# Optimization experiments

Hardware: AMD Instinct MI355X
Metric: run time of the kernel (lower is better)

## Reference

```python
import jax, jax.numpy as jnp
import numpy as np
import math

CAPACITY_FACTOR = 1.0

def setup_inputs() -> dict:
    key = jax.random.key(0)
    k1, k2 = jax.random.split(key)
    x = jax.random.normal(k1, (8192, 2048), dtype=jnp.float32)
    wg = jax.random.normal(k2, (64, 2048), dtype=jnp.float32) * (1.0 / np.sqrt(2048))
    return {"x": x, "wg": wg}

def reference(x, wg):
    # logits = Linear(model_dim, num_experts, bias=False)(x)
    logits = jnp.einsum('sd,ed->se', x, wg)
    gates = jax.nn.softmax(logits, axis=1)  # [s, e]
    s, e = gates.shape
    capacity = math.ceil(s / e * CAPACITY_FACTOR)  # static
    indices1_s = jnp.argmax(gates, axis=1)  # [s]
    mask1 = jax.nn.one_hot(indices1_s, e, dtype=jnp.int32)  # [s, e]
    locations1 = jnp.cumsum(mask1, axis=0) - 1  # position within each expert queue
    # aux load-balancing loss
    me = jnp.mean(gates, axis=0)
    ce = jnp.mean(mask1.astype(gates.dtype), axis=0)
    l_aux = jnp.mean(me * ce) * (e * e)
    # drop tokens over capacity
    mask1 = mask1 * (locations1 < capacity).astype(jnp.int32)
    locations1_s = jnp.sum(locations1 * mask1, axis=1)  # [s] int
    mask1_float = mask1.astype(gates.dtype)
    gates1_s = jnp.sum(gates * mask1_float, axis=1)  # 'se,se->s'
    gates1 = gates1_s[:, None] * mask1_float         # 's,se->se'
    locations1_sc = jax.nn.one_hot(locations1_s, capacity, dtype=gates.dtype)  # [s, c]
    combine_weights = gates1[:, :, None] * locations1_sc[:, None, :]  # 'se,sc->sec'
    dispatch_mask = combine_weights.astype(bool)
    return l_aux, combine_weights, dispatch_mask
```

## Files before the change

### kernel.cpp

```cpp
#include <hip/hip_runtime.h>
#include <cstdint>
#include <cstddef>


#define S_TOK 8192
#define NEXP 64
#define DIM 2048
#define CAP 128
#define COMB_ELEMS ((size_t)S_TOK * NEXP * CAP)
#define OUT_ELEMS (1 + 2 * COMB_ELEMS)
#define NQUAD (OUT_ELEMS / 4)

#define TOK_TILE 128
#define NSLICE 4
#define KSLICE (DIM / NSLICE)
#define KC 32

#define GEMM_BLKS 256
#define ZERO_BLKS 768
#define TOTAL_BLKS (GEMM_BLKS + ZERO_BLKS)
#define QCHUNK 43691

__global__ __launch_bounds__(256, 4) void fused_zero_gemm(
    const float* __restrict__ x, const float* __restrict__ wg,
    float* __restrict__ P, float* __restrict__ gsum,
    float* __restrict__ out)
{
    const int tid = threadIdx.x;

    if (blockIdx.x >= GEMM_BLKS) {
        const int zb = blockIdx.x - GEMM_BLKS;
        size_t begin = (size_t)zb * QCHUNK;
        size_t end   = begin + QCHUNK;
        if (end > (size_t)NQUAD) end = (size_t)NQUAD;
        const float4 z = { 0.0f, 0.0f, 0.0f, 0.0f };
        for (size_t q = begin + tid; q < end; q += 256)
            *(float4*)(out + 4 * q) = z;
        if (zb == 0 && tid == 0) out[OUT_ELEMS - 1] = 0.0f;
        return;
    }

    __shared__ float xs[KC][132];
    __shared__ float wsh[KC][68];

    const int tile  = blockIdx.x >> 2;
    const int slice = blockIdx.x & 3;
    const int tok0 = tile * TOK_TILE;
    const int k0   = slice * KSLICE;

    if (blockIdx.x == 0 && tid < NEXP) gsum[tid] = 0.0f;

    const int tt = tid >> 4;
    const int te = tid & 15;

    float acc[8][4];
#pragma unroll
    for (int i = 0; i < 8; ++i)
#pragma unroll
        for (int j = 0; j < 4; ++j) acc[i][j] = 0.0f;

    const int we  = tid & 63;
    const int wkq = tid >> 6;

    float4 xv[4], wv[2];
#pragma unroll
    for (int r = 0; r < 4; ++r) {
        int idx = tid + 256 * r;
        int t = idx >> 3, kq = idx & 7;
        xv[r] = *(const float4*)(x + (size_t)(tok0 + t) * DIM + k0 + 4 * kq);
    }
    wv[0] = *(const float4*)(wg + (size_t)we * DIM + k0 + 4 * wkq);
    wv[1] = *(const float4*)(wg + (size_t)we * DIM + k0 + 4 * (wkq + 4));

    for (int kc = 0; kc < KSLICE; kc += KC) {
        __syncthreads();
#pragma unroll
        for (int r = 0; r < 4; ++r) {
            int idx = tid + 256 * r;
            int t = idx >> 3, k4 = (idx & 7) * 4;
            xs[k4 + 0][t] = xv[r].x; xs[k4 + 1][t] = xv[r].y;
            xs[k4 + 2][t] = xv[r].z; xs[k4 + 3][t] = xv[r].w;
        }
        {
            int k4 = 4 * wkq;
            wsh[k4 + 0][we] = wv[0].x; wsh[k4 + 1][we] = wv[0].y;
            wsh[k4 + 2][we] = wv[0].z; wsh[k4 + 3][we] = wv[0].w;
            int k4b = k4 + 16;
            wsh[k4b + 0][we] = wv[1].x; wsh[k4b + 1][we] = wv[1].y;
            wsh[k4b + 2][we] = wv[1].z; wsh[k4b + 3][we] = wv[1].w;
        }
        __syncthreads();
        if (kc + KC < KSLICE) {
#pragma unroll
            for (int r = 0; r < 4; ++r) {
                int idx = tid + 256 * r;
                int t = idx >> 3, kq = idx & 7;
                xv[r] = *(const float4*)(x + (size_t)(tok0 + t) * DIM + k0 + kc + KC + 4 * kq);
            }
            wv[0] = *(const float4*)(wg + (size_t)we * DIM + k0 + kc + KC + 4 * wkq);
            wv[1] = *(const float4*)(wg + (size_t)we * DIM + k0 + kc + KC + 4 * (wkq + 4));
        }
#pragma unroll 8
        for (int k = 0; k < KC; ++k) {
            float4 a0 = *(const float4*)&xs[k][8 * tt];
            float4 a1 = *(const float4*)&xs[k][8 * tt + 4];
            float4 b  = *(const float4*)&wsh[k][4 * te];
            const float* ap0 = &a0.x; const float* ap1 = &a1.x; const float* bp = &b.x;
#pragma unroll
            for (int i = 0; i < 4; ++i)
#pragma unroll
                for (int j = 0; j < 4; ++j) {
                    acc[i][j]     += ap0[i] * bp[j];
                    acc[i + 4][j] += ap1[i] * bp[j];
                }
        }
    }

#pragma unroll
    for (int i = 0; i < 8; ++i) {
        size_t off = ((size_t)slice * S_TOK + tok0 + 8 * tt + i) * NEXP + 4 * te;
        float4 v = { acc[i][0], acc[i][1], acc[i][2], acc[i][3] };
        *(float4*)(P + off) = v;
    }
}

__global__ __launch_bounds__(256) void reduce_kernel(
    const float* __restrict__ P,
    int* __restrict__ idx_out, float* __restrict__ gate_out,
    float* __restrict__ gsum)
{
    __shared__ float sme[NEXP];
    const int tid = threadIdx.x;
    const int tok0 = blockIdx.x * 32;
    const int ty = tid >> 5;
    const int tx = tid & 31;
    const int t0 = ty * 4;
    const int e0 = tx * 2;

    if (tid < NEXP) sme[tid] = 0.0f;

    float gm0 = 0.0f, gm1 = 0.0f;
#pragma unroll
    for (int i = 0; i < 4; ++i) {
        int tok = tok0 + t0 + i;
        float l0 = 0.0f, l1 = 0.0f;
#pragma unroll
        for (int s = 0; s < NSLICE; ++s) {
            float2 p = *(const float2*)&P[((size_t)s * S_TOK + tok) * NEXP + e0];
            l0 += p.x; l1 += p.y;
        }
        float v; int ix;
        if (l1 > l0) { v = l1; ix = e0 + 1; } else { v = l0; ix = e0; }
#pragma unroll
        for (int off = 16; off; off >>= 1) {
            float ov = __shfl_xor(v, off, 32);
            int   oi = __shfl_xor(ix, off, 32);
            if (ov > v || (ov == v && oi < ix)) { v = ov; ix = oi; }
        }
        float z0 = __expf(l0 - v), z1 = __expf(l1 - v);
        float zs = z0 + z1;
#pragma unroll
        for (int off = 16; off; off >>= 1) zs += __shfl_xor(zs, off, 32);
        float inv = 1.0f / zs;
        gm0 += z0 * inv; gm1 += z1 * inv;
        if (tx == 0) {
            idx_out[tok]  = ix;
            gate_out[tok] = inv;
        }
    }
    atomicAdd(&sme[e0], gm0);
    atomicAdd(&sme[e0 + 1], gm1);
    __syncthreads();
    if (tid < NEXP) atomicAdd(&gsum[tid], sme[tid]);
}

__global__ __launch_bounds__(1024) void scan_scatter(
    const int* __restrict__ idx, const float* __restrict__ gate,
    const float* __restrict__ gsum, float* __restrict__ out)
{
    __shared__ int wavecnt[16][NEXP];
    __shared__ int basecnt[NEXP];
    const int tid  = threadIdx.x;
    const int lane = tid & 63;
    const int wv   = tid >> 6;

    if (tid < NEXP) basecnt[tid] = 0;
    __syncthreads();

    for (int it = 0; it < S_TOK / 1024; ++it) {
        int tok = it * 1024 + tid;
        int e = idx[tok];
        unsigned long long m = ~0ull, lm = ~0ull;
#pragma unroll
        for (int b = 0; b < 6; ++b) {
            unsigned long long bal = __ballot((e >> b) & 1);
            m  &= ((e >> b) & 1)    ? bal : ~bal;
            lm &= ((lane >> b) & 1) ? bal : ~bal;
        }
        int rank = __popcll(m & ((1ull << lane) - 1ull));
        wavecnt[wv][lane] = __popcll(lm);
        __syncthreads();
        int off = 0;
        for (int w = 0; w < wv; ++w) off += wavecnt[w][e];
        int loc = basecnt[e] + off + rank;
        if (loc < CAP) {
            size_t base = 1 + (size_t)tok * (NEXP * CAP) + (size_t)e * CAP + loc;
            out[base] = gate[tok];
            out[base + COMB_ELEMS] = 1.0f;
        }
        __syncthreads();
        if (tid < NEXP) {
            int tot = 0;
#pragma unroll
            for (int w = 0; w < 16; ++w) tot += wavecnt[w][tid];
            basecnt[tid] += tot;
        }
        __syncthreads();
    }

    if (tid < NEXP) {
        float p = gsum[tid] * (float)basecnt[tid];
#pragma unroll
        for (int off = 32; off; off >>= 1) p += __shfl_xor(p, off, 64);
        if (tid == 0) out[0] = p * 9.5367431640625e-07f;
    }
}

extern "C" void kernel_launch(void* const* d_in, const int* in_sizes, int n_in,
                              void* d_out, int out_size, void* d_ws, size_t ws_size,
                              hipStream_t stream) {
    const float* x  = (const float*)d_in[0];
    const float* wg = (const float*)d_in[1];
    float* out = (float*)d_out;

    int*   idx  = (int*)d_ws;
    float* gate = (float*)((char*)d_ws + 32768);
    float* gsum = (float*)((char*)d_ws + 65536);
    float* P    = (float*)((char*)d_ws + 262144);

    fused_zero_gemm<<<TOTAL_BLKS, 256, 0, stream>>>(x, wg, P, gsum, out);
    reduce_kernel<<<S_TOK / 32, 256, 0, stream>>>(P, idx, gate, gsum);
    scan_scatter<<<1, 1024, 0, stream>>>(idx, gate, gsum, out);
}
```

Measured before the change: 615.6 us.

## Spread output zeroing across all three kernels and split scatter out of scan

The large output memset was done only inside the GEMM kernel. It is now split into three ranges, each handled by extra blocks in the gemm, reduce and scan kernels, so the zero-fill overlaps the small compute stages, including the single-block scan. The scan now writes per-token locations to workspace, and a separate scatter kernel writes the nonzero entries after all zeroing has finished. This removes the ordering hazard between zeroing and scattering, at the cost of one more launch and a small extra buffer.

```diff
diff --git a/kernel.cpp b/kernel.cpp
--- a/kernel.cpp
+++ b/kernel.cpp
@@ -9,33 +9,36 @@
 #define CAP 128
 #define COMB_ELEMS ((size_t)S_TOK * NEXP * CAP)
 #define OUT_ELEMS (1 + 2 * COMB_ELEMS)
-#define NQUAD (OUT_ELEMS / 4)
+#define NQUAD ((size_t)(OUT_ELEMS / 4))
+
+#define QA ((size_t)14000000)
+#define QB ((size_t)24000000)
 
 #define TOK_TILE 128
 #define NSLICE 4
 #define KSLICE (DIM / NSLICE)
 #define KC 32
 
-#define GEMM_BLKS 256
-#define ZERO_BLKS 768
-#define TOTAL_BLKS (GEMM_BLKS + ZERO_BLKS)
-#define QCHUNK 43691
-
-__global__ __launch_bounds__(256, 4) void fused_zero_gemm(
+__device__ __forceinline__ void zero_quads(float* __restrict__ out,
+                                           size_t q_begin, size_t q_end,
+                                           int nblocks, int bid) {
+    const float4 z = { 0.0f, 0.0f, 0.0f, 0.0f };
+    size_t stride = (size_t)nblocks * blockDim.x;
+    for (size_t q = q_begin + (size_t)bid * blockDim.x + threadIdx.x;
+         q < q_end; q += stride)
+        *(float4*)(out + 4 * q) = z;
+}
+
+__global__ __launch_bounds__(256, 4) void gemm_zero_a(
     const float* __restrict__ x, const float* __restrict__ wg,
     float* __restrict__ P, float* __restrict__ gsum,
     float* __restrict__ out)
 {
     const int tid = threadIdx.x;
 
-    if (blockIdx.x >= GEMM_BLKS) {
-        const int zb = blockIdx.x - GEMM_BLKS;
-        size_t begin = (size_t)zb * QCHUNK;
-        size_t end   = begin + QCHUNK;
-        if (end > (size_t)NQUAD) end = (size_t)NQUAD;
-        const float4 z = { 0.0f, 0.0f, 0.0f, 0.0f };
-        for (size_t q = begin + tid; q < end; q += 256)
-            *(float4*)(out + 4 * q) = z;
+    if (blockIdx.x >= 256) {
+        const int zb = blockIdx.x - 256;
+        zero_quads(out, 0, QA, 768, zb);
         if (zb == 0 && tid == 0) out[OUT_ELEMS - 1] = 0.0f;
         return;
     }
@@ -124,13 +127,19 @@
     }
 }
 
-__global__ __launch_bounds__(256) void reduce_kernel(
+__global__ __launch_bounds__(256) void reduce_zero_b(
     const float* __restrict__ P,
     int* __restrict__ idx_out, float* __restrict__ gate_out,
-    float* __restrict__ gsum)
-{
+    float* __restrict__ gsum, float* __restrict__ out)
+{
+    const int tid = threadIdx.x;
+
+    if (blockIdx.x >= 256) {
+        zero_quads(out, QA, QB, 768, blockIdx.x - 256);
+        return;
+    }
+
     __shared__ float sme[NEXP];
-    const int tid = threadIdx.x;
     const int tok0 = blockIdx.x * 32;
     const int ty = tid >> 5;
     const int tx = tid & 31;
@@ -174,13 +183,19 @@
     if (tid < NEXP) atomicAdd(&gsum[tid], sme[tid]);
 }
 
-__global__ __launch_bounds__(1024) void scan_scatter(
-    const int* __restrict__ idx, const float* __restrict__ gate,
-    const float* __restrict__ gsum, float* __restrict__ out)
-{
+__global__ __launch_bounds__(1024) void scan_zero_c(
+    const int* __restrict__ idx, const float* __restrict__ gsum,
+    int* __restrict__ loc_out, float* __restrict__ out)
+{
+    const int tid = threadIdx.x;
+
+    if (blockIdx.x > 0) {
+        zero_quads(out, QB, NQUAD, 256, (int)blockIdx.x - 1);
+        return;
+    }
+
     __shared__ int wavecnt[16][NEXP];
     __shared__ int basecnt[NEXP];
-    const int tid  = threadIdx.x;
     const int lane = tid & 63;
     const int wv   = tid >> 6;
 
@@ -202,12 +217,7 @@
         __syncthreads();
         int off = 0;
         for (int w = 0; w < wv; ++w) off += wavecnt[w][e];
-        int loc = basecnt[e] + off + rank;
-        if (loc < CAP) {
-            size_t base = 1 + (size_t)tok * (NEXP * CAP) + (size_t)e * CAP + loc;
-            out[base] = gate[tok];
-            out[base + COMB_ELEMS] = 1.0f;
-        }
+        loc_out[tok] = basecnt[e] + off + rank;
         __syncthreads();
         if (tid < NEXP) {
             int tot = 0;
@@ -223,6 +233,19 @@
 #pragma unroll
         for (int off = 32; off; off >>= 1) p += __shfl_xor(p, off, 64);
         if (tid == 0) out[0] = p * 9.5367431640625e-07f;
+    }
+}
+
+__global__ __launch_bounds__(256) void scatter_kernel(
+    const int* __restrict__ idx, const float* __restrict__ gate,
+    const int* __restrict__ loc, float* __restrict__ out)
+{
+    int t = blockIdx.x * 256 + threadIdx.x;
+    int l = loc[t];
+    if (l < CAP) {
+        size_t base = 1 + (size_t)t * (NEXP * CAP) + (size_t)idx[t] * CAP + l;
+        out[base] = gate[t];
+        out[base + COMB_ELEMS] = 1.0f;
     }
 }
 
@@ -236,9 +259,11 @@
     int*   idx  = (int*)d_ws;
     float* gate = (float*)((char*)d_ws + 32768);
     float* gsum = (float*)((char*)d_ws + 65536);
+    int*   loc  = (int*)((char*)d_ws + 66560);
     float* P    = (float*)((char*)d_ws + 262144);
 
-    fused_zero_gemm<<<TOTAL_BLKS, 256, 0, stream>>>(x, wg, P, gsum, out);
-    reduce_kernel<<<S_TOK / 32, 256, 0, stream>>>(P, idx, gate, gsum);
-    scan_scatter<<<1, 1024, 0, stream>>>(idx, gate, gsum, out);
-}
+    gemm_zero_a<<<1024, 256, 0, stream>>>(x, wg, P, gsum, out);
+    reduce_zero_b<<<1024, 256, 0, stream>>>(P, idx, gate, gsum, out);
+    scan_zero_c<<<257, 1024, 0, stream>>>(idx, gsum, loc, out);
+    scatter_kernel<<<S_TOK / 256, 256, 0, stream>>>(idx, gate, loc, out);
+}
```

After: 591.6 us. 3.9% less time.
